# Optimization experiments

Measured on AMD Instinct MI355X. Metric: run time of the kernel, lower is better.

## Reference

```python
import jax, jax.numpy as jnp
import numpy as np


def setup_inputs() -> dict:
    key = jax.random.key(0)
    k1, k2, k3 = jax.random.split(key, 3)
    B, N = 4096, 1024
    src = jax.random.normal(k1, (B, 3, N), dtype=jnp.float32)
    src_corr = jax.random.normal(k2, (B, 3, N), dtype=jnp.float32)
    weight = jax.random.uniform(k3, (B, 1, N), dtype=jnp.float32)
    return {"src": src, "src_corr": src_corr, "weight": weight}


def reference(src, src_corr, weight):
    # src, src_corr: (B, 3, N); weight: (B, 1, N)
    wsum = weight.sum(axis=2, keepdims=True)                      # (B,1,1)
    src2 = (src * weight).sum(axis=2, keepdims=True) / wsum       # (B,3,1) weighted centroid
    corr2 = (src_corr * weight).sum(axis=2, keepdims=True) / wsum  # (B,3,1)
    src_c = src - src2
    corr_c = src_corr - corr2
    # weighted 3x3 covariance H = (src_c * w) @ corr_c^T
    H = jnp.einsum('bin,bjn->bij', src_c * weight, corr_c)        # (B,3,3)
    u, s, vh = jnp.linalg.svd(H, full_matrices=False)
    v = jnp.swapaxes(vh, -1, -2)                                   # (B,3,3)
    ut = jnp.swapaxes(u, -1, -2)
    det = jnp.linalg.det(v @ ut)                                   # (B,)
    # R = v @ diag(1,1,det) @ u^T  -> scale last column of v by det
    v_adj = v.at[:, :, 2].multiply(det[:, None])
    R = v_adj @ ut                                                 # (B,3,3)
    t = -jnp.matmul(R, src2) + corr2                               # (B,3,1)
    return R, t
```

## Files before the change

kernel.cpp:

```cpp
#include <hip/hip_runtime.h>
#include <math.h>


__device__ __forceinline__ float wred(float v) {
#pragma unroll
    for (int o = 32; o > 0; o >>= 1) v += __shfl_down(v, o);
    return v;
}

__global__ __launch_bounds__(256) void wsvd_reduce(
    const float* __restrict__ src, const float* __restrict__ corr,
    const float* __restrict__ wgt, float* __restrict__ sums)
{
    const int wave = threadIdx.x >> 6;
    const int lane = threadIdx.x & 63;
    const int b = blockIdx.x * 4 + wave;

    const float4* W = reinterpret_cast<const float4*>(wgt  + (size_t)b * 1024);
    const float4* S = reinterpret_cast<const float4*>(src  + (size_t)b * 3072);
    const float4* C = reinterpret_cast<const float4*>(corr + (size_t)b * 3072);

    float wsum = 0.f, ws0 = 0.f, ws1 = 0.f, ws2 = 0.f;
    float wc0 = 0.f, wc1 = 0.f, wc2 = 0.f;
    float m00 = 0.f, m01 = 0.f, m02 = 0.f;
    float m10 = 0.f, m11 = 0.f, m12 = 0.f;
    float m20 = 0.f, m21 = 0.f, m22 = 0.f;

#pragma unroll
    for (int k = 0; k < 4; ++k) {
        const int idx = lane + 64 * k;
        float4 wv = W[idx];
        float4 a0 = S[idx], a1 = S[idx + 256], a2 = S[idx + 512];
        float4 b0 = C[idx], b1 = C[idx + 256], b2 = C[idx + 512];
#define PROC(f) { \
        float w_ = wv.f; \
        float t0 = w_ * a0.f, t1 = w_ * a1.f, t2 = w_ * a2.f; \
        wsum += w_; ws0 += t0; ws1 += t1; ws2 += t2; \
        wc0 += w_ * b0.f; wc1 += w_ * b1.f; wc2 += w_ * b2.f; \
        m00 += t0 * b0.f; m01 += t0 * b1.f; m02 += t0 * b2.f; \
        m10 += t1 * b0.f; m11 += t1 * b1.f; m12 += t1 * b2.f; \
        m20 += t2 * b0.f; m21 += t2 * b1.f; m22 += t2 * b2.f; }
        PROC(x) PROC(y) PROC(z) PROC(w)
#undef PROC
    }

    wsum = wred(wsum);
    ws0 = wred(ws0); ws1 = wred(ws1); ws2 = wred(ws2);
    wc0 = wred(wc0); wc1 = wred(wc1); wc2 = wred(wc2);
    m00 = wred(m00); m01 = wred(m01); m02 = wred(m02);
    m10 = wred(m10); m11 = wred(m11); m12 = wred(m12);
    m20 = wred(m20); m21 = wred(m21); m22 = wred(m22);

    if (lane == 0) {
        float4* o = reinterpret_cast<float4*>(sums + (size_t)b * 16);
        o[0] = make_float4(wsum, ws0, ws1, ws2);
        o[1] = make_float4(wc0, wc1, wc2, m00);
        o[2] = make_float4(m01, m02, m10, m11);
        o[3] = make_float4(m12, m20, m21, m22);
    }
}

__global__ __launch_bounds__(256) void wsvd_solve(
    const float* __restrict__ sums, float* __restrict__ R_out,
    float* __restrict__ t_out, int B)
{
    const int b = blockIdx.x * blockDim.x + threadIdx.x;
    if (b >= B) return;

    const float4* p = reinterpret_cast<const float4*>(sums + (size_t)b * 16);
    float4 q0 = p[0], q1 = p[1], q2 = p[2], q3 = p[3];

    double wsum = q0.x;
    double ws0 = q0.y, ws1 = q0.z, ws2 = q0.w;
    double wc0 = q1.x, wc1 = q1.y, wc2 = q1.z;
    double m00 = q1.w, m01 = q2.x, m02 = q2.y;
    double m10 = q2.z, m11 = q2.w, m12 = q3.x;
    double m20 = q3.y, m21 = q3.z, m22 = q3.w;

    double inv = 1.0 / wsum;
    double s2x = ws0 * inv, s2y = ws1 * inv, s2z = ws2 * inv;
    double c2x = wc0 * inv, c2y = wc1 * inv, c2z = wc2 * inv;
    double h00 = m00 - ws0 * wc0 * inv, h01 = m01 - ws0 * wc1 * inv, h02 = m02 - ws0 * wc2 * inv;
    double h10 = m10 - ws1 * wc0 * inv, h11 = m11 - ws1 * wc1 * inv, h12 = m12 - ws1 * wc2 * inv;
    double h20 = m20 - ws2 * wc0 * inv, h21 = m21 - ws2 * wc1 * inv, h22 = m22 - ws2 * wc2 * inv;

    double a00 = h00 * h00 + h10 * h10 + h20 * h20;
    double a11 = h01 * h01 + h11 * h11 + h21 * h21;
    double a22 = h02 * h02 + h12 * h12 + h22 * h22;
    double a01 = h00 * h01 + h10 * h11 + h20 * h21;
    double a02 = h00 * h02 + h10 * h12 + h20 * h22;
    double a12 = h01 * h02 + h11 * h12 + h21 * h22;

    double v00 = 1.0, v01 = 0.0, v02 = 0.0;
    double v10 = 0.0, v11 = 1.0, v12 = 0.0;
    double v20 = 0.0, v21 = 0.0, v22 = 1.0;

#define ROT(app, aqq, apq, apr, aqr, vp0, vq0, vp1, vq1, vp2, vq2) { \
    double apq_ = apq; \
    double cc, ss, tt; \
    if (fabs(apq_) > 1e-300) { \
        double tau = (aqq - app) / (2.0 * apq_); \
        tt = copysign(1.0, tau) / (fabs(tau) + sqrt(1.0 + tau * tau)); \
        cc = 1.0 / sqrt(1.0 + tt * tt); ss = tt * cc; \
    } else { tt = 0.0; cc = 1.0; ss = 0.0; } \
    app -= tt * apq_; aqq += tt * apq_; apq = 0.0; \
    { double pr = apr, qr = aqr; apr = cc * pr - ss * qr; aqr = ss * pr + cc * qr; } \
    { double t0_ = vp0; vp0 = cc * t0_ - ss * vq0; vq0 = ss * t0_ + cc * vq0; } \
    { double t0_ = vp1; vp1 = cc * t0_ - ss * vq1; vq1 = ss * t0_ + cc * vq1; } \
    { double t0_ = vp2; vp2 = cc * t0_ - ss * vq2; vq2 = ss * t0_ + cc * vq2; } }

    for (int sweep = 0; sweep < 6; ++sweep) {
        ROT(a00, a11, a01, a02, a12, v00, v01, v10, v11, v20, v21)
        ROT(a00, a22, a02, a01, a12, v00, v02, v10, v12, v20, v22)
        ROT(a11, a22, a12, a01, a02, v01, v02, v11, v12, v21, v22)
    }
#undef ROT

    double l0 = a00, l1 = a11, l2 = a22;
#define CSWAP(li, lj, x0, y0, x1, y1, x2, y2) if (li < lj) { double t_; \
    t_ = li; li = lj; lj = t_; t_ = x0; x0 = y0; y0 = t_; \
    t_ = x1; x1 = y1; y1 = t_; t_ = x2; x2 = y2; y2 = t_; }
    CSWAP(l0, l1, v00, v01, v10, v11, v20, v21)
    CSWAP(l0, l2, v00, v02, v10, v12, v20, v22)
    CSWAP(l1, l2, v01, v02, v11, v12, v21, v22)
#undef CSWAP

    double u0x = h00 * v00 + h01 * v10 + h02 * v20;
    double u0y = h10 * v00 + h11 * v10 + h12 * v20;
    double u0z = h20 * v00 + h21 * v10 + h22 * v20;
    double n0 = sqrt(u0x * u0x + u0y * u0y + u0z * u0z);
    if (n0 > 1e-300) { double r = 1.0 / n0; u0x *= r; u0y *= r; u0z *= r; }
    else { u0x = 1.0; u0y = 0.0; u0z = 0.0; }

    double u1x = h00 * v01 + h01 * v11 + h02 * v21;
    double u1y = h10 * v01 + h11 * v11 + h12 * v21;
    double u1z = h20 * v01 + h21 * v11 + h22 * v21;
    double dp = u0x * u1x + u0y * u1y + u0z * u1z;
    u1x -= dp * u0x; u1y -= dp * u0y; u1z -= dp * u0z;
    double n1 = sqrt(u1x * u1x + u1y * u1y + u1z * u1z);
    if (n1 > 1e-300) { double r = 1.0 / n1; u1x *= r; u1y *= r; u1z *= r; }
    else {
        if (fabs(u0x) < 0.9) { u1x = 0.0; u1y = u0z; u1z = -u0y; }
        else                 { u1x = -u0z; u1y = 0.0; u1z = u0x; }
        double r = 1.0 / sqrt(u1x * u1x + u1y * u1y + u1z * u1z);
        u1x *= r; u1y *= r; u1z *= r;
    }

    double u2x = u0y * u1z - u0z * u1y;
    double u2y = u0z * u1x - u0x * u1z;
    double u2z = u0x * u1y - u0y * u1x;

    double detV = v00 * (v11 * v22 - v12 * v21)
                - v01 * (v10 * v22 - v12 * v20)
                + v02 * (v10 * v21 - v11 * v20);
    double d = (detV >= 0.0) ? 1.0 : -1.0;

    double r00 = v00 * u0x + v01 * u1x + d * v02 * u2x;
    double r01 = v00 * u0y + v01 * u1y + d * v02 * u2y;
    double r02 = v00 * u0z + v01 * u1z + d * v02 * u2z;
    double r10 = v10 * u0x + v11 * u1x + d * v12 * u2x;
    double r11 = v10 * u0y + v11 * u1y + d * v12 * u2y;
    double r12 = v10 * u0z + v11 * u1z + d * v12 * u2z;
    double r20 = v20 * u0x + v21 * u1x + d * v22 * u2x;
    double r21 = v20 * u0y + v21 * u1y + d * v22 * u2y;
    double r22 = v20 * u0z + v21 * u1z + d * v22 * u2z;

    double tx = c2x - (r00 * s2x + r01 * s2y + r02 * s2z);
    double ty = c2y - (r10 * s2x + r11 * s2y + r12 * s2z);
    double tz = c2z - (r20 * s2x + r21 * s2y + r22 * s2z);

    float* Ro = R_out + (size_t)b * 9;
    Ro[0] = (float)r00; Ro[1] = (float)r01; Ro[2] = (float)r02;
    Ro[3] = (float)r10; Ro[4] = (float)r11; Ro[5] = (float)r12;
    Ro[6] = (float)r20; Ro[7] = (float)r21; Ro[8] = (float)r22;
    float* To = t_out + (size_t)b * 3;
    To[0] = (float)tx; To[1] = (float)ty; To[2] = (float)tz;
}

extern "C" void kernel_launch(void* const* d_in, const int* in_sizes, int n_in,
                              void* d_out, int out_size, void* d_ws, size_t ws_size,
                              hipStream_t stream) {
    const float* src  = (const float*)d_in[0];
    const float* corr = (const float*)d_in[1];
    const float* wgt  = (const float*)d_in[2];
    float* out = (float*)d_out;

    const int N = 1024;
    const int B = in_sizes[2] / N;
    float* sums = (float*)d_ws;

    wsvd_reduce<<<B / 4, 256, 0, stream>>>(src, corr, wgt, sums);
    wsvd_solve<<<(B + 255) / 256, 256, 0, stream>>>(sums, out, out + (size_t)B * 9, B);
}
```

Before: 141.4 us.

## Use one block per batch in reduce, smaller solve blocks, fewer Jacobi sweeps

The reduction kernel now gives each batch a full 256-thread block instead of a single wave. Each thread loads one float4 chunk, and the four per-wave partial sums are combined through shared memory. This raises the number of independent loads in flight per batch and the block count, at the cost of a __syncthreads and a shared-memory pass per block. The solve kernel now launches 64-thread blocks so more CUs take part. Its Jacobi loop drops from 6 to 5 sweeps, which cuts fp64 work but could slightly reduce SVD accuracy.

```diff
diff --git a/kernel.cpp b/kernel.cpp
--- a/kernel.cpp
+++ b/kernel.cpp
@@ -2,7 +2,7 @@
 #include <math.h>
 
 
-__device__ __forceinline__ float wred(float v) {
+__device__ __forceinline__ float wred64(float v) {
 #pragma unroll
     for (int o = 32; o > 0; o >>= 1) v += __shfl_down(v, o);
     return v;
@@ -12,13 +12,17 @@
     const float* __restrict__ src, const float* __restrict__ corr,
     const float* __restrict__ wgt, float* __restrict__ sums)
 {
-    const int wave = threadIdx.x >> 6;
-    const int lane = threadIdx.x & 63;
-    const int b = blockIdx.x * 4 + wave;
+    const int b = blockIdx.x;
+    const int t = threadIdx.x;
+    const int wave = t >> 6, lane = t & 63;
 
     const float4* W = reinterpret_cast<const float4*>(wgt  + (size_t)b * 1024);
     const float4* S = reinterpret_cast<const float4*>(src  + (size_t)b * 3072);
     const float4* C = reinterpret_cast<const float4*>(corr + (size_t)b * 3072);
+
+    float4 wv = W[t];
+    float4 a0 = S[t], a1 = S[t + 256], a2 = S[t + 512];
+    float4 b0 = C[t], b1 = C[t + 256], b2 = C[t + 512];
 
     float wsum = 0.f, ws0 = 0.f, ws1 = 0.f, ws2 = 0.f;
     float wc0 = 0.f, wc1 = 0.f, wc2 = 0.f;
@@ -26,41 +30,40 @@
     float m10 = 0.f, m11 = 0.f, m12 = 0.f;
     float m20 = 0.f, m21 = 0.f, m22 = 0.f;
 
-#pragma unroll
-    for (int k = 0; k < 4; ++k) {
-        const int idx = lane + 64 * k;
-        float4 wv = W[idx];
-        float4 a0 = S[idx], a1 = S[idx + 256], a2 = S[idx + 512];
-        float4 b0 = C[idx], b1 = C[idx + 256], b2 = C[idx + 512];
 #define PROC(f) { \
-        float w_ = wv.f; \
-        float t0 = w_ * a0.f, t1 = w_ * a1.f, t2 = w_ * a2.f; \
-        wsum += w_; ws0 += t0; ws1 += t1; ws2 += t2; \
-        wc0 += w_ * b0.f; wc1 += w_ * b1.f; wc2 += w_ * b2.f; \
-        m00 += t0 * b0.f; m01 += t0 * b1.f; m02 += t0 * b2.f; \
-        m10 += t1 * b0.f; m11 += t1 * b1.f; m12 += t1 * b2.f; \
-        m20 += t2 * b0.f; m21 += t2 * b1.f; m22 += t2 * b2.f; }
-        PROC(x) PROC(y) PROC(z) PROC(w)
+    float w_ = wv.f; \
+    float t0 = w_ * a0.f, t1 = w_ * a1.f, t2 = w_ * a2.f; \
+    wsum += w_; ws0 += t0; ws1 += t1; ws2 += t2; \
+    wc0 += w_ * b0.f; wc1 += w_ * b1.f; wc2 += w_ * b2.f; \
+    m00 += t0 * b0.f; m01 += t0 * b1.f; m02 += t0 * b2.f; \
+    m10 += t1 * b0.f; m11 += t1 * b1.f; m12 += t1 * b2.f; \
+    m20 += t2 * b0.f; m21 += t2 * b1.f; m22 += t2 * b2.f; }
+    PROC(x) PROC(y) PROC(z) PROC(w)
 #undef PROC
+
+    wsum = wred64(wsum);
+    ws0 = wred64(ws0); ws1 = wred64(ws1); ws2 = wred64(ws2);
+    wc0 = wred64(wc0); wc1 = wred64(wc1); wc2 = wred64(wc2);
+    m00 = wred64(m00); m01 = wred64(m01); m02 = wred64(m02);
+    m10 = wred64(m10); m11 = wred64(m11); m12 = wred64(m12);
+    m20 = wred64(m20); m21 = wred64(m21); m22 = wred64(m22);
+
+    __shared__ float sm[4][16];
+    if (lane == 0) {
+        float* o = sm[wave];
+        o[0] = wsum; o[1] = ws0; o[2] = ws1; o[3] = ws2;
+        o[4] = wc0;  o[5] = wc1; o[6] = wc2; o[7] = m00;
+        o[8] = m01;  o[9] = m02; o[10] = m10; o[11] = m11;
+        o[12] = m12; o[13] = m20; o[14] = m21; o[15] = m22;
     }
-
-    wsum = wred(wsum);
-    ws0 = wred(ws0); ws1 = wred(ws1); ws2 = wred(ws2);
-    wc0 = wred(wc0); wc1 = wred(wc1); wc2 = wred(wc2);
-    m00 = wred(m00); m01 = wred(m01); m02 = wred(m02);
-    m10 = wred(m10); m11 = wred(m11); m12 = wred(m12);
-    m20 = wred(m20); m21 = wred(m21); m22 = wred(m22);
-
-    if (lane == 0) {
-        float4* o = reinterpret_cast<float4*>(sums + (size_t)b * 16);
-        o[0] = make_float4(wsum, ws0, ws1, ws2);
-        o[1] = make_float4(wc0, wc1, wc2, m00);
-        o[2] = make_float4(m01, m02, m10, m11);
-        o[3] = make_float4(m12, m20, m21, m22);
+    __syncthreads();
+    if (t < 16) {
+        float s = sm[0][t] + sm[1][t] + sm[2][t] + sm[3][t];
+        sums[(size_t)b * 16 + t] = s;
     }
 }
 
-__global__ __launch_bounds__(256) void wsvd_solve(
+__global__ __launch_bounds__(64) void wsvd_solve(
     const float* __restrict__ sums, float* __restrict__ R_out,
     float* __restrict__ t_out, int B)
 {
@@ -109,7 +112,7 @@
     { double t0_ = vp1; vp1 = cc * t0_ - ss * vq1; vq1 = ss * t0_ + cc * vq1; } \
     { double t0_ = vp2; vp2 = cc * t0_ - ss * vq2; vq2 = ss * t0_ + cc * vq2; } }
 
-    for (int sweep = 0; sweep < 6; ++sweep) {
+    for (int sweep = 0; sweep < 5; ++sweep) {
         ROT(a00, a11, a01, a02, a12, v00, v01, v10, v11, v20, v21)
         ROT(a00, a22, a02, a01, a12, v00, v02, v10, v12, v20, v22)
         ROT(a11, a22, a12, a01, a02, v01, v02, v11, v12, v21, v22)
@@ -189,6 +192,6 @@
     const int B = in_sizes[2] / N;
     float* sums = (float*)d_ws;
 
-    wsvd_reduce<<<B / 4, 256, 0, stream>>>(src, corr, wgt, sums);
-    wsvd_solve<<<(B + 255) / 256, 256, 0, stream>>>(sums, out, out + (size_t)B * 9, B);
+    wsvd_reduce<<<B, 256, 0, stream>>>(src, corr, wgt, sums);
+    wsvd_solve<<<(B + 63) / 64, 64, 0, stream>>>(sums, out, out + (size_t)B * 9, B);
 }
```

New measurement: 141.2 us. About the same (-0.2%).
